# Kernel optimization log

Hardware: AMD Instinct MI355X
Metric: run time of the kernel (lower is better)

Reference implementation:

```python
import jax, jax.numpy as jnp
import numpy as np
from jax import lax

LAYERS = 4
B, C, D1, D2, D3, D4 = 2, 3, 48, 48, 48, 24

_DN = lax.ConvDimensionNumbers(lhs_spec=(0, 1, 2, 3, 4, 5),
                               rhs_spec=(0, 1, 2, 3, 4, 5),
                               out_spec=(0, 1, 2, 3, 4, 5))


def conv4d(x, w, b, pad):
    # x: (B, Cin, D1, D2, D3, D4); w: (Cout, Cin, k1, k2, k3, k4); pad: 4-tuple
    y = lax.conv_general_dilated(x, w, window_strides=(1, 1, 1, 1),
                                 padding=[(p, p) for p in pad],
                                 dimension_numbers=_DN)
    return y + b.reshape(1, -1, 1, 1, 1, 1)


def setup_inputs() -> dict:
    key = jax.random.key(0)
    ks = jax.random.split(key, 10)
    s = 0.05
    return {
        "f": jax.random.normal(ks[0], (B, C, D1, D2, D3, D4), jnp.float32),
        "bondary": jax.random.normal(ks[1], (B, C, D1, D2, D3, D4), jnp.float32),
        "Wg": jax.random.normal(ks[2], (LAYERS, 3, 6, 3, 3, 3, 3), jnp.float32) * s,
        "bg": jax.random.normal(ks[3], (LAYERS, 3), jnp.float32) * s,
        "W1": jax.random.normal(ks[4], (LAYERS, 3, 3, 3, 3, 3, 1), jnp.float32) * s,
        "b1": jax.random.normal(ks[5], (LAYERS, 3), jnp.float32) * s,
        "W2": jax.random.normal(ks[6], (LAYERS, 3, 3, 1, 1, 1, 3), jnp.float32) * s,
        "b2": jax.random.normal(ks[7], (LAYERS, 3), jnp.float32) * s,
        "Wd": jax.random.normal(ks[8], (LAYERS, 3, 3, 1, 1, 1, 1), jnp.float32) * s,
        "bd": jax.random.normal(ks[9], (LAYERS, 3), jnp.float32) * s,
    }


def reference(f, bondary, Wg, bg, W1, b1, W2, b2, Wd, bd):
    out = f
    for i in range(LAYERS):
        temp = jnp.concatenate((out, bondary), axis=1)          # (B, 6, ...)
        temp = conv4d(temp, Wg[i], bg[i], (1, 1, 1, 1))          # gather
        temp = conv4d(temp, W1[i], b1[i], (1, 1, 1, 0))          # (3,3,3,1)
        out = conv4d(temp, W2[i], b2[i], (0, 0, 0, 1)) \
            + conv4d(out, Wd[i], bd[i], (0, 0, 0, 0))            # residual
    return out
```

## Files before the change

kernel.cpp:

```cpp
#include <hip/hip_runtime.h>

typedef _Float16 half2_t __attribute__((ext_vector_type(2)));
typedef unsigned int uint32;

#if __has_builtin(__builtin_amdgcn_fdot2)
#define FDOT2(a, b, c) __builtin_amdgcn_fdot2((a), (b), (c), false)
#else
__device__ __forceinline__ float FDOT2(half2_t a, half2_t b, float c) {
    return c + (float)a.x * (float)b.x + (float)a.y * (float)b.y;
}
#endif

__device__ __forceinline__ half2_t h2_from_bits(uint32 b) {
    union { uint32 u; half2_t h; } c; c.u = b; return c.h;
}
__device__ __forceinline__ uint32 bits_from_h2(half2_t h) {
    union { uint32 u; half2_t h; } c; c.h = h; return c.u;
}

namespace {
constexpr int D  = 48;
constexpr int D4 = 24;
constexpr int S2 = D * D4;
constexpr int S1 = D * S2;
constexpr int SC = D * S1;
constexpr int NB = 2;
constexpr int NELEM = NB * 3 * SC;
constexpr int NPAIR_H2 = NB * 3 * SC;
constexpr int NS = NB * D * D * D;
}


__global__ __launch_bounds__(256) void pack_weights(
        const float* __restrict__ Wg, half2_t* __restrict__ pw)
{
    int i = blockIdx.x * 256 + threadIdx.x;
    const int NTOT = 4 * 3 * 27 * 9;
    if (i >= NTOT) return;
    int k4 = i % 3; int r = i / 3;
    int co = r % 3; r /= 3;
    int k123 = r % 27; r /= 27;
    int p = r % 3; int l = r / 3;
    int ciA = 2 * p, ciB = 2 * p + 1;
    float a = Wg[((l * 3 + co) * 6 + ciA) * 81 + k123 * 3 + k4];
    float b = Wg[((l * 3 + co) * 6 + ciB) * 81 + k123 * 3 + k4];
    pw[i] = half2_t{(_Float16)a, (_Float16)b};
}

__global__ __launch_bounds__(256) void pack_init(
        const float* __restrict__ f, const float* __restrict__ bnd,
        half2_t* __restrict__ pairs)
{
    int i = blockIdx.x * 256 + threadIdx.x;
    int plane = i / (SC / 4);
    int zz = (i % (SC / 4)) * 4;
    int b = plane / 3, p = plane % 3;
    const float* A; const float* Bc;
    if (p == 0)      { A = f   + (size_t)(b*3 + 0) * SC; Bc = f   + (size_t)(b*3 + 1) * SC; }
    else if (p == 1) { A = f   + (size_t)(b*3 + 2) * SC; Bc = bnd + (size_t)(b*3 + 0) * SC; }
    else             { A = bnd + (size_t)(b*3 + 1) * SC; Bc = bnd + (size_t)(b*3 + 2) * SC; }
    float4 a = *(const float4*)(A + zz);
    float4 c = *(const float4*)(Bc + zz);
    union { float4 f4; half2_t h[4]; } u;
    u.h[0] = half2_t{(_Float16)a.x, (_Float16)c.x};
    u.h[1] = half2_t{(_Float16)a.y, (_Float16)c.y};
    u.h[2] = half2_t{(_Float16)a.z, (_Float16)c.z};
    u.h[3] = half2_t{(_Float16)a.w, (_Float16)c.w};
    *(float4*)(pairs + (size_t)plane * SC + zz) = u.f4;
}


__global__ __launch_bounds__(256, 4) void convA(
        const half2_t* __restrict__ pairs, const half2_t* __restrict__ pw,
        const float* __restrict__ bg, _Float16* __restrict__ dst)
{
    int t = blockIdx.x * 256 + threadIdx.x;
    int H = t & 1;
    int s = t >> 1;
    int x3 = s % D; int r = s / D;
    int x2 = r % D; r /= D;
    int x1 = r % D; int b = r / D;

    const uint32 maskL = H ? 0xFFFFFFFFu : 0u;
    const uint32 maskR = ~maskL;
    const int bodyOff = 12 * H;
    const int edgeOff = 12 - H;

    float acc[3][12];
#pragma unroll
    for (int c = 0; c < 3; ++c) {
        float bb = bg[c];
#pragma unroll
        for (int j = 0; j < 12; ++j) acc[c][j] = bb;
    }

#pragma unroll 1
    for (int p = 0; p < 3; ++p) {
        const half2_t* src = pairs + (size_t)(b*3 + p) * SC;
#pragma unroll 1
        for (int k1 = 0; k1 < 3; ++k1) {
            int z1 = x1 + k1 - 1;
            if ((unsigned)z1 >= (unsigned)D) continue;
            const half2_t* src1 = src + z1 * S1;
#pragma unroll
            for (int k2 = 0; k2 < 3; ++k2) {
                int z2 = x2 + k2 - 1;
                if ((unsigned)z2 >= (unsigned)D) continue;
#pragma unroll
                for (int k3 = 0; k3 < 3; ++k3) {
                    int z3 = x3 + k3 - 1;
                    if ((unsigned)z3 >= (unsigned)D) continue;
                    const half2_t* lb = src1 + z2 * S2 + z3 * D4;
                    union { float4 f4[3]; half2_t h[12]; } B;
                    const float4* L4 = (const float4*)(lb + bodyOff);
                    B.f4[0] = L4[0]; B.f4[1] = L4[1]; B.f4[2] = L4[2];
                    uint32 ev = *(const uint32*)(lb + edgeOff);

                    half2_t W[14];
                    W[0]  = h2_from_bits(ev & maskL);
#pragma unroll
                    for (int i = 0; i < 12; ++i) W[1 + i] = B.h[i];
                    W[13] = h2_from_bits(ev & maskR);

                    const half2_t* w = pw + (size_t)((p * 27 + (k1*9 + k2*3 + k3)) * 9);
#pragma unroll
                    for (int co = 0; co < 3; ++co) {
                        half2_t w0 = w[co*3 + 0];
                        half2_t w1 = w[co*3 + 1];
                        half2_t w2 = w[co*3 + 2];
#pragma unroll
                        for (int j = 0; j < 12; ++j) {
                            float a = acc[co][j];
                            a = FDOT2(w0, W[j],     a);
                            a = FDOT2(w1, W[j + 1], a);
                            a = FDOT2(w2, W[j + 2], a);
                            acc[co][j] = a;
                        }
                    }
                }
            }
        }
    }

    int spos = x1 * S1 + x2 * S2 + x3 * D4 + 12 * H;
#pragma unroll
    for (int co = 0; co < 3; ++co) {
        union { float2 f2[3]; _Float16 h[12]; } u;
#pragma unroll
        for (int j = 0; j < 12; ++j) u.h[j] = (_Float16)acc[co][j];
        float2* o2 = (float2*)(dst + (b*3 + co) * (size_t)SC + spos);
#pragma unroll
        for (int q = 0; q < 3; ++q) o2[q] = u.f2[q];
    }
}


__global__ __launch_bounds__(256, 3) void convBC(
        const _Float16* __restrict__ t1, half2_t* pairs,
        const float* __restrict__ W1, const float* __restrict__ b1,
        const float* __restrict__ W2, const float* __restrict__ b2,
        const float* __restrict__ Wd, const float* __restrict__ bd,
        float* __restrict__ dstF32, int writeF32)
{
    int t = blockIdx.x * 256 + threadIdx.x;
    int H = t & 1;
    int s = t >> 1;
    int x3 = s % D; int r = s / D;
    int x2 = r % D; r /= D;
    int x1 = r % D; int b = r / D;
    const bool isH1 = (H != 0);

    int spos = x1 * S1 + x2 * S2 + x3 * D4;
    const int bodyOff = 12 * H;
    const int edgeOff = 12 - H;

    float t2l[3][14];
#pragma unroll
    for (int c = 0; c < 3; ++c) {
        float bb = b1[c];
        t2l[c][0]  = isH1 ? bb : 0.f;
        t2l[c][13] = isH1 ? 0.f : bb;
#pragma unroll
        for (int m = 1; m < 13; ++m) t2l[c][m] = bb;
    }

#pragma unroll 1
    for (int ci = 0; ci < 3; ++ci) {
        const _Float16* src = t1 + (b*3 + ci) * (size_t)SC;
#pragma unroll 1
        for (int k1 = 0; k1 < 3; ++k1) {
            int z1 = x1 + k1 - 1;
            if ((unsigned)z1 >= (unsigned)D) continue;
            const _Float16* src1 = src + z1 * S1;
#pragma unroll
            for (int k2 = 0; k2 < 3; ++k2) {
                int z2 = x2 + k2 - 1;
                if ((unsigned)z2 >= (unsigned)D) continue;
#pragma unroll
                for (int k3 = 0; k3 < 3; ++k3) {
                    int z3 = x3 + k3 - 1;
                    if ((unsigned)z3 >= (unsigned)D) continue;
                    const _Float16* lb = src1 + z2 * S2 + z3 * D4;
                    union { float2 f2[3]; half2_t h[6]; } Bd;
                    const float2* L2 = (const float2*)(lb + bodyOff);
                    Bd.f2[0] = L2[0]; Bd.f2[1] = L2[1]; Bd.f2[2] = L2[2];
                    _Float16 eh = lb[edgeOff];
                    float ef = (float)eh;

                    float v[14];
                    v[0]  = isH1 ? ef : 0.f;
                    v[13] = isH1 ? 0.f : ef;
#pragma unroll
                    for (int i = 0; i < 6; ++i) {
                        v[1 + 2*i] = (float)Bd.h[i].x;
                        v[2 + 2*i] = (float)Bd.h[i].y;
                    }
                    int kk = k1*9 + k2*3 + k3;
                    float wA = W1[  0 + ci*27 + kk];
                    float wB = W1[ 81 + ci*27 + kk];
                    float wC = W1[162 + ci*27 + kk];
#pragma unroll
                    for (int m = 0; m < 14; ++m) {
                        t2l[0][m] += wA * v[m];
                        t2l[1][m] += wB * v[m];
                        t2l[2][m] += wC * v[m];
                    }
                }
            }
        }
    }

    half2_t* p0ptr = pairs + (size_t)(b*3 + 0) * SC + spos + 12*H;
    half2_t* p1ptr = pairs + (size_t)(b*3 + 1) * SC + spos + 12*H;
    half2_t rp0[12], rp1[12];
#pragma unroll
    for (int q = 0; q < 3; ++q) {
        union { float4 f4; half2_t h[4]; } u;
        u.f4 = ((const float4*)p0ptr)[q];
        rp0[4*q+0]=u.h[0]; rp0[4*q+1]=u.h[1]; rp0[4*q+2]=u.h[2]; rp0[4*q+3]=u.h[3];
        u.f4 = ((const float4*)p1ptr)[q];
        rp1[4*q+0]=u.h[0]; rp1[4*q+1]=u.h[1]; rp1[4*q+2]=u.h[2]; rp1[4*q+3]=u.h[3];
    }

    float U[3][3][3];
#pragma unroll
    for (int co = 0; co < 3; ++co)
#pragma unroll
        for (int ci = 0; ci < 3; ++ci)
#pragma unroll
            for (int k = 0; k < 3; ++k)
                U[co][ci][k] = W2[co*9 + ci*3 + k];
    float WD[9];
#pragma unroll
    for (int i = 0; i < 9; ++i) WD[i] = Wd[i];
    float c0 = b2[0] + bd[0], c1 = b2[1] + bd[1], c2 = b2[2] + bd[2];

    float o0[12], o1[12], o2[12];
#pragma unroll
    for (int n = 0; n < 12; ++n) {
        float s0 = c0, s1 = c1, s2 = c2;
#pragma unroll
        for (int ci = 0; ci < 3; ++ci) {
            float tm = t2l[ci][n + 0];
            float tc = t2l[ci][n + 1];
            float tp = t2l[ci][n + 2];
            s0 += U[0][ci][0]*tm + U[0][ci][1]*tc + U[0][ci][2]*tp;
            s1 += U[1][ci][0]*tm + U[1][ci][1]*tc + U[1][ci][2]*tp;
            s2 += U[2][ci][0]*tm + U[2][ci][1]*tc + U[2][ci][2]*tp;
        }
        float pv0 = (float)rp0[n].x, pv1 = (float)rp0[n].y, pv2 = (float)rp1[n].x;
        s0 += WD[0]*pv0 + WD[1]*pv1 + WD[2]*pv2;
        s1 += WD[3]*pv0 + WD[4]*pv1 + WD[5]*pv2;
        s2 += WD[6]*pv0 + WD[7]*pv1 + WD[8]*pv2;
        o0[n] = s0; o1[n] = s1; o2[n] = s2;
    }

    {
        union { float4 f4[3]; half2_t h[12]; } u0, u1;
#pragma unroll
        for (int n = 0; n < 12; ++n) {
            u0.h[n] = half2_t{(_Float16)o0[n], (_Float16)o1[n]};
            u1.h[n] = half2_t{(_Float16)o2[n], rp1[n].y};
        }
#pragma unroll
        for (int q = 0; q < 3; ++q) {
            ((float4*)p0ptr)[q] = u0.f4[q];
            ((float4*)p1ptr)[q] = u1.f4[q];
        }
    }

    if (writeF32) {
        float* d0 = dstF32 + (size_t)(b*3 + 0) * SC + spos + 12*H;
        float* d1 = dstF32 + (size_t)(b*3 + 1) * SC + spos + 12*H;
        float* d2 = dstF32 + (size_t)(b*3 + 2) * SC + spos + 12*H;
#pragma unroll
        for (int q = 0; q < 3; ++q) {
            ((float4*)d0)[q] = make_float4(o0[4*q], o0[4*q+1], o0[4*q+2], o0[4*q+3]);
            ((float4*)d1)[q] = make_float4(o1[4*q], o1[4*q+1], o1[4*q+2], o1[4*q+3]);
            ((float4*)d2)[q] = make_float4(o2[4*q], o2[4*q+1], o2[4*q+2], o2[4*q+3]);
        }
    }
}

extern "C" void kernel_launch(void* const* d_in, const int* in_sizes, int n_in,
                              void* d_out, int out_size, void* d_ws, size_t ws_size,
                              hipStream_t stream)
{
    const float* f   = (const float*)d_in[0];
    const float* bnd = (const float*)d_in[1];
    const float* Wg  = (const float*)d_in[2];
    const float* bg  = (const float*)d_in[3];
    const float* W1  = (const float*)d_in[4];
    const float* b1  = (const float*)d_in[5];
    const float* W2  = (const float*)d_in[6];
    const float* b2  = (const float*)d_in[7];
    const float* Wd  = (const float*)d_in[8];
    const float* bd  = (const float*)d_in[9];

    _Float16* t1h   = (_Float16*)d_ws;
    half2_t*  pairs = (half2_t*)(t1h + NELEM);
    half2_t*  pw    = pairs + NPAIR_H2;

    pack_weights<<<dim3((2916 + 255) / 256), dim3(256), 0, stream>>>(Wg, pw);
    pack_init<<<dim3(NB * 3 * (SC / 4) / 256), dim3(256), 0, stream>>>(f, bnd, pairs);

    const int grid = 2 * NS / 256;
    for (int l = 0; l < 4; ++l) {
        convA<<<dim3(grid), dim3(256), 0, stream>>>(pairs, pw + l * 729, bg + l*3, t1h);
        convBC<<<dim3(grid), dim3(256), 0, stream>>>(
            t1h, pairs, W1 + l*243, b1 + l*3, W2 + l*27, b2 + l*3,
            Wd + l*9, bd + l*3, (float*)d_out, l == 3 ? 1 : 0);
    }
}
```

Baseline: 1.072 ms.

## Stage halo tiles of input pairs in LDS for 3x3x3x3 gather conv

```diff
diff --git a/kernel.cpp b/kernel.cpp
--- a/kernel.cpp
+++ b/kernel.cpp
@@ -13,9 +13,6 @@
 
 __device__ __forceinline__ half2_t h2_from_bits(uint32 b) {
     union { uint32 u; half2_t h; } c; c.u = b; return c.h;
-}
-__device__ __forceinline__ uint32 bits_from_h2(half2_t h) {
-    union { uint32 u; half2_t h; } c; c.h = h; return c.u;
 }
 
 namespace {
@@ -28,6 +25,13 @@
 constexpr int NELEM = NB * 3 * SC;
 constexpr int NPAIR_H2 = NB * 3 * SC;
 constexpr int NS = NB * D * D * D;
+
+constexpr int T1 = 8, T2 = 4, T3 = 4;
+constexpr int HL1 = T1 + 2, HL2 = T2 + 2, HL3 = T3 + 2;
+constexpr int NLINE = HL1 * HL2 * HL3;
+constexpr int LSTR  = 28;
+constexpr int NT1 = D / T1, NT2 = D / T2, NT3 = D / T3;
+constexpr int TILES = NT1 * NT2 * NT3;
 }
 
 
@@ -74,17 +78,28 @@
         const half2_t* __restrict__ pairs, const half2_t* __restrict__ pw,
         const float* __restrict__ bg, _Float16* __restrict__ dst)
 {
-    int t = blockIdx.x * 256 + threadIdx.x;
-    int H = t & 1;
-    int s = t >> 1;
-    int x3 = s % D; int r = s / D;
-    int x2 = r % D; r /= D;
-    int x1 = r % D; int b = r / D;
+    __shared__ half2_t lds[NLINE * LSTR];
+
+    int tid = threadIdx.x;
+    int H  = tid & 1;
+    int li = tid >> 1;
+    int l3 = li & 3;
+    int l2 = (li >> 2) & 3;
+    int l1 = li >> 4;
+
+    int bid = blockIdx.x;
+    int b   = bid / TILES;
+    int rr  = bid % TILES;
+    int t1i = rr / (NT2 * NT3);
+    int t2i = (rr / NT3) % NT2;
+    int t3i = rr % NT3;
+
+    int x1 = t1i * T1 + l1;
+    int x2 = t2i * T2 + l2;
+    int x3 = t3i * T3 + l3;
 
     const uint32 maskL = H ? 0xFFFFFFFFu : 0u;
     const uint32 maskR = ~maskL;
-    const int bodyOff = 12 * H;
-    const int edgeOff = 12 - H;
 
     float acc[3][12];
 #pragma unroll
@@ -94,27 +109,44 @@
         for (int j = 0; j < 12; ++j) acc[c][j] = bb;
     }
 
+    const int baseline = (l1 * HL2 + l2) * HL3 + l3;
+    const half2_t* lbase = &lds[baseline * LSTR];
+
 #pragma unroll 1
     for (int p = 0; p < 3; ++p) {
-        const half2_t* src = pairs + (size_t)(b*3 + p) * SC;
-#pragma unroll 1
+        if (p) __syncthreads();
+        {
+            const half2_t* src = pairs + (size_t)(b*3 + p) * SC;
+            for (int i = tid; i < NLINE * 6; i += 256) {
+                int q = i % 6; int line = i / 6;
+                int s3 = line % HL3;
+                int s2 = (line / HL3) % HL2;
+                int s1 = line / (HL2 * HL3);
+                int z1 = t1i * T1 - 1 + s1;
+                int z2 = t2i * T2 - 1 + s2;
+                int z3 = t3i * T3 - 1 + s3;
+                float4 val = make_float4(0.f, 0.f, 0.f, 0.f);
+                if ((unsigned)z1 < (unsigned)D && (unsigned)z2 < (unsigned)D &&
+                    (unsigned)z3 < (unsigned)D)
+                    val = *(const float4*)(src + (size_t)z1*S1 + z2*S2 + z3*D4 + q*4);
+                *(float4*)(&lds[line * LSTR + q * 4]) = val;
+            }
+        }
+        __syncthreads();
+
+        const half2_t* pwp = pw + (size_t)p * 243;
+#pragma unroll
         for (int k1 = 0; k1 < 3; ++k1) {
-            int z1 = x1 + k1 - 1;
-            if ((unsigned)z1 >= (unsigned)D) continue;
-            const half2_t* src1 = src + z1 * S1;
 #pragma unroll
             for (int k2 = 0; k2 < 3; ++k2) {
-                int z2 = x2 + k2 - 1;
-                if ((unsigned)z2 >= (unsigned)D) continue;
 #pragma unroll
                 for (int k3 = 0; k3 < 3; ++k3) {
-                    int z3 = x3 + k3 - 1;
-                    if ((unsigned)z3 >= (unsigned)D) continue;
-                    const half2_t* lb = src1 + z2 * S2 + z3 * D4;
+                    const half2_t* lb = lbase +
+                        (k1 * (HL2*HL3) + k2 * HL3 + k3) * LSTR;
                     union { float4 f4[3]; half2_t h[12]; } B;
-                    const float4* L4 = (const float4*)(lb + bodyOff);
+                    const float4* L4 = (const float4*)(lb + 12 * H);
                     B.f4[0] = L4[0]; B.f4[1] = L4[1]; B.f4[2] = L4[2];
-                    uint32 ev = *(const uint32*)(lb + edgeOff);
+                    uint32 ev = *(const uint32*)(lb + (12 - H));
 
                     half2_t W[14];
                     W[0]  = h2_from_bits(ev & maskL);
@@ -122,7 +154,7 @@
                     for (int i = 0; i < 12; ++i) W[1 + i] = B.h[i];
                     W[13] = h2_from_bits(ev & maskR);
 
-                    const half2_t* w = pw + (size_t)((p * 27 + (k1*9 + k2*3 + k3)) * 9);
+                    const half2_t* w = pwp + (size_t)(k1*9 + k2*3 + k3) * 9;
 #pragma unroll
                     for (int co = 0; co < 3; ++co) {
                         half2_t w0 = w[co*3 + 0];
@@ -324,10 +356,11 @@
     pack_weights<<<dim3((2916 + 255) / 256), dim3(256), 0, stream>>>(Wg, pw);
     pack_init<<<dim3(NB * 3 * (SC / 4) / 256), dim3(256), 0, stream>>>(f, bnd, pairs);
 
-    const int grid = 2 * NS / 256;
+    const int gridA  = NB * TILES;
+    const int gridBC = 2 * NS / 256;
     for (int l = 0; l < 4; ++l) {
-        convA<<<dim3(grid), dim3(256), 0, stream>>>(pairs, pw + l * 729, bg + l*3, t1h);
-        convBC<<<dim3(grid), dim3(256), 0, stream>>>(
+        convA<<<dim3(gridA), dim3(256), 0, stream>>>(pairs, pw + l * 729, bg + l*3, t1h);
+        convBC<<<dim3(gridBC), dim3(256), 0, stream>>>(
             t1h, pairs, W1 + l*243, b1 + l*3, W2 + l*27, b2 + l*3,
             Wd + l*9, bd + l*3, (float*)d_out, l == 3 ? 1 : 0);
     }
```

New measurement: 1.053 ms. No clear change (-1.8%).
